# Performance work log

Hardware: AMD Instinct MI355X
Metric: run time of the kernel (lower is better)

The kernel has to match this reference:

```python
import jax, jax.numpy as jnp
import numpy as np

# ---- static skeleton configuration ----
TOPOLOGY = [[0,1],[1,2],[2,3],[3,4],[0,5],[5,6],[6,7],[7,8],[0,9],[9,10],[10,11],[11,12],
            [12,13],[13,14],[12,15],[15,16],[16,17],[17,18],[18,19],[12,20],[20,21],[21,22],[22,23],[23,24]]
NEIGHBOUR_LIST = [[0,1,2,4,5,8,9,24],[0,1,2,3,4,8],[0,1,2,3],[1,2,3],[0,1,4,5,6,8,9,24],[0,4,5,6,7,8],
                  [4,5,6,7],[5,6,7],[0,1,4,5,8,9,10,24],[0,4,8,9,10,11],[8,9,10,11,12,14,19],
                  [9,10,11,12,13,14,15,19,20],[10,11,12,13,14,15,19,20],[11,12,13,14,19],
                  [10,11,12,13,14,15,16,19,20],[11,12,14,15,16,17,19],[14,15,16,17,18],[15,16,17,18],
                  [16,17,18],[10,11,12,13,14,15,19,20,21],[11,12,14,19,20,21,22],[19,20,21,22,23],
                  [20,21,22,23],[21,22,23],[0,4,8,24]]
JOINT_NUM, IN_C, OUT_C, K, STRIDE, PAD = 25, 200, 400, 3, 2, 1
GN_GROUPS, GN_EPS = 10, 1e-5

def build_mask(nbr_list, in_c, out_c, joint_num, k):
    cin, cout = in_c // joint_num, out_c // joint_num
    m = np.zeros((out_c, in_c, k), np.float32)
    for i, nbr in enumerate(nbr_list):
        cols = [j * cin + c for j in nbr for c in range(cin)]
        m[i * cout:(i + 1) * cout, cols, :] = 1.0
    return jnp.asarray(m)

def build_pool(edges, cpe):
    edge_num = len(edges) + 1
    deg = {}
    for a, b in edges:
        deg[a] = deg.get(a, 0) + 1; deg[b] = deg.get(b, 0) + 1
    seq_list = []
    def find_seq(j, seq):
        if deg[j] > 2 and j != 0:
            seq_list.append(seq); seq = []
        if deg[j] == 1:
            seq_list.append(seq); return
        for idx, (a, b) in enumerate(edges):
            if a == j:
                find_seq(b, seq + [idx])
    find_seq(0, [])
    pooling_list = []
    for seq in seq_list:
        if len(seq) % 2 == 1:
            pooling_list.append([seq[0]]); seq = seq[1:]
        for i in range(0, len(seq), 2):
            pooling_list.append([seq[i], seq[i + 1]])
    pooling_list.append([edge_num - 1])
    W = np.zeros((len(pooling_list) * cpe, edge_num * cpe), np.float32)
    for i, pair in enumerate(pooling_list):
        for j in pair:
            W[i * cpe:(i + 1) * cpe, j * cpe:(j + 1) * cpe] += np.eye(cpe, dtype=np.float32) / len(pair)
    return jnp.asarray(W)

MASK0 = build_mask(NEIGHBOUR_LIST, IN_C, IN_C, JOINT_NUM, K)    # extra conv in->in
MASK1 = build_mask(NEIGHBOUR_LIST, IN_C, OUT_C, JOINT_NUM, K)   # main conv in->out
MASK_SC = build_mask(NEIGHBOUR_LIST, IN_C, OUT_C, JOINT_NUM, 1) # shortcut k=1
POOL_W = build_pool(TOPOLOGY, OUT_C // JOINT_NUM)               # [224, 400]

def conv1d(x, w, b, stride, pad):
    if pad > 0:
        x = jnp.pad(x, ((0, 0), (0, 0), (pad, pad)), mode='reflect')
    y = jax.lax.conv_general_dilated(x, w, (stride,), 'VALID',
                                     dimension_numbers=('NCH', 'OIH', 'NCH'))
    return y + b[None, :, None]

def group_norm(x, gamma, beta):
    B, C, T = x.shape
    xg = x.reshape(B, GN_GROUPS, C // GN_GROUPS, T)
    mu = xg.mean((2, 3), keepdims=True)
    var = xg.var((2, 3), keepdims=True)
    xn = ((xg - mu) * jax.lax.rsqrt(var + GN_EPS)).reshape(B, C, T)
    return xn * gamma[None, :, None] + beta[None, :, None]

def prelu(x, a):
    return jnp.where(x >= 0, x, a[0] * x)

def setup_inputs() -> dict:
    key = jax.random.key(0)
    ks = jax.random.split(key, 8)
    return {
        'x': jax.random.normal(ks[0], (16, IN_C, 8192), jnp.float32),
        'w0': jax.random.normal(ks[1], (IN_C, IN_C, K), jnp.float32) * 0.05,
        'b0': jax.random.normal(ks[2], (IN_C,), jnp.float32) * 0.05,
        'a0': jnp.full((1,), 0.25, jnp.float32),
        'w1': jax.random.normal(ks[3], (OUT_C, IN_C, K), jnp.float32) * 0.05,
        'b1': jax.random.normal(ks[4], (OUT_C,), jnp.float32) * 0.05,
        'gn_gamma': jnp.ones((OUT_C,), jnp.float32),
        'gn_beta': jnp.zeros((OUT_C,), jnp.float32),
        'ws': jax.random.normal(ks[5], (OUT_C, IN_C, 1), jnp.float32) * 0.05,
        'bs': jax.random.normal(ks[6], (OUT_C,), jnp.float32) * 0.05,
        'a1': jnp.full((1,), 0.25, jnp.float32),
    }

def reference(x, w0, b0, a0, w1, b1, gn_gamma, gn_beta, ws, bs, a1):
    # residual branch: extra SkeletonConv + PReLU, SkeletonConv (stride 2), GroupNorm
    h = conv1d(x, w0 * MASK0, b0, 1, PAD)
    h = prelu(h, a0)
    h = conv1d(h, w1 * MASK1, b1, STRIDE, PAD)
    h = group_norm(h, gn_gamma, gn_beta)
    # shortcut: masked 1x1 conv, stride 2
    s = conv1d(x, ws * MASK_SC, bs, STRIDE, 0)
    out = h + s                                   # [B, 400, 4096]
    out = jnp.einsum('nc,bct->bnt', POOL_W, out)  # SkeletonPool mean -> [B, 224, 4096]
    return prelu(out, a1)
```

## Files before the change

### kernel.cpp

```cpp
#include <hip/hip_runtime.h>

#define BATCH 16
#define CIN   200
#define T1    8192
#define COUTC 400
#define TT2   4096
#define NJ    25
#define NGROUP 10
#define CPG   40
#define NPOOL 14
#define CROWB 528

typedef __attribute__((ext_vector_type(8))) short bf16x8;
typedef __attribute__((ext_vector_type(4))) float f32x4;

__constant__ int NBR_OFF[NJ + 1] = {0,8,14,18,21,29,35,39,42,50,56,63,72,80,85,94,101,106,110,113,122,129,134,138,141,145};
__constant__ int NBR[145] = {
 0,1,2,4,5,8,9,24,
 0,1,2,3,4,8,
 0,1,2,3,
 1,2,3,
 0,1,4,5,6,8,9,24,
 0,4,5,6,7,8,
 4,5,6,7,
 5,6,7,
 0,1,4,5,8,9,10,24,
 0,4,8,9,10,11,
 8,9,10,11,12,14,19,
 9,10,11,12,13,14,15,19,20,
 10,11,12,13,14,15,19,20,
 11,12,13,14,19,
 10,11,12,13,14,15,16,19,20,
 11,12,14,15,16,17,19,
 14,15,16,17,18,
 15,16,17,18,
 16,17,18,
 10,11,12,13,14,15,19,20,21,
 11,12,14,19,20,21,22,
 19,20,21,22,23,
 20,21,22,23,
 21,22,23,
 0,4,8,24};
__constant__ int PAIR_A[NPOOL] = {0,2,4,6,8,10,12,14,15,17,19,20,22,24};
__constant__ int PAIR_B[NPOOL] = {1,3,5,7,9,11,13,-1,16,18,-1,21,23,-1};
__constant__ int JSPLIT8[9] = {0,3,6,9,12,15,18,21,25};
__constant__ int QPB[4] = {0,4,7,10};
__constant__ int QPE[4] = {4,7,10,14};
__constant__ int PUOFF[15] = {0,9,13,22,26,35,45,53,62,70,74,83,91,95,99};
__constant__ int PU[99] = {
 0,1,2,3,4,5,8,9,24,
 0,1,2,3,
 0,1,4,5,6,7,8,9,24,
 4,5,6,7,
 0,1,4,5,8,9,10,11,24,
 8,9,10,11,12,13,14,15,19,20,
 10,11,12,13,14,15,19,20,
 10,11,12,13,14,15,16,19,20,
 11,12,14,15,16,17,18,19,
 15,16,17,18,
 10,11,12,13,14,15,19,20,21,
 11,12,14,19,20,21,22,23,
 20,21,22,23,
 0,4,8,24};
__constant__ int PNMF[NPOOL] = {7,3,7,3,7,8,6,7,6,3,7,6,3,3};
__constant__ int FB0[NPOOL]  = {0,7,10,17,20,27,35,41,48,54,57,64,70,73};
__constant__ int FRAG_P[76] = {
 0,0,0,0,0,0,0, 1,1,1, 2,2,2,2,2,2,2, 3,3,3, 4,4,4,4,4,4,4, 5,5,5,5,5,5,5,5,
 6,6,6,6,6,6, 7,7,7,7,7,7,7, 8,8,8,8,8,8, 9,9,9, 10,10,10,10,10,10,10,
 11,11,11,11,11,11, 12,12,12, 13,13,13};
__constant__ int NSF[NJ] = {2,2,1,1,2,2,1,1,2,2,2,3,2,2,3,2,2,1,1,3,2,2,1,1,1};
__constant__ int FBS[NJ] = {0,2,4,5,6,8,10,11,12,14,16,18,21,23,25,28,30,32,33,34,37,39,41,42,43};
__constant__ int FRAG_SJ[44] = {
 0,0, 1,1, 2, 3, 4,4, 5,5, 6, 7, 8,8, 9,9, 10,10, 11,11,11, 12,12, 13,13,
 14,14,14, 15,15, 16,16, 17, 18, 19,19,19, 20,20, 21,21, 22, 23, 24};
#define NF1   (NJ * 7)
#define DSC_SC   304
#define DSC_C1   480
#define DSC_TOT  (DSC_C1 + NF1 * 4)

__device__ __forceinline__ unsigned bfround(float f) {
    unsigned u = __builtin_bit_cast(unsigned, f);
    return (u + 0x7FFFu + ((u >> 16) & 1u)) >> 16;
}
__device__ __forceinline__ unsigned packbf(float lo, float hi) {
    return bfround(lo) | (bfround(hi) << 16);
}
__device__ __forceinline__ float bflo(unsigned u) { return __builtin_bit_cast(float, u << 16); }
__device__ __forceinline__ float bfhi(unsigned u) { return __builtin_bit_cast(float, u & 0xFFFF0000u); }

__global__ void prep_all(const float* __restrict__ w1, const float* __restrict__ w0,
                         const float* __restrict__ wsc,
                         unsigned short* __restrict__ wA1, unsigned short* __restrict__ wA0,
                         unsigned short* __restrict__ wAs, int* __restrict__ dsc)
{
    const int bid = blockIdx.x;
    if (bid < NF1) {
        const int f  = bid;
        const int jo = f / 7;
        const int mf = f - jo * 7;
        const int off = NBR_OFF[jo];
        const int deg = NBR_OFF[jo + 1] - off;
        for (int e = threadIdx.x; e < 512; e += 256) {
            int lane = e >> 3, j = e & 7;
            int m = lane & 15, kb = lane >> 4;
            int c8 = mf * 4 + kb;
            float v = 0.f;
            if (c8 < 3 * deg) {
                int tap = (c8 >= 2 * deg) ? 2 : ((c8 >= deg) ? 1 : 0);
                int nbr_i = c8 - tap * deg;
                int ci = NBR[off + nbr_i] * 8 + j;
                v = w1[(size_t)(jo * 16 + m) * 600 + ci * 3 + tap];
            }
            wA1[(size_t)f * 512 + e] = (unsigned short)bfround(v);
        }
    } else if (bid < NF1 + 76) {
        const int f  = bid - NF1;
        const int p  = FRAG_P[f];
        const int mf = f - FB0[p];
        const int puo = PUOFF[p];
        const int u   = PUOFF[p + 1] - puo;
        for (int e = threadIdx.x; e < 512; e += 256) {
            int lane = e >> 3, j = e & 7;
            int m = lane & 15, kb = lane >> 4;
            int c8 = mf * 4 + kb;
            int jm = (m < 8) ? PAIR_A[p] : PAIR_B[p];
            float v = 0.f;
            if (c8 < 3 * u && jm >= 0) {
                int tap = (c8 >= 2 * u) ? 2 : ((c8 >= u) ? 1 : 0);
                int ni  = c8 - tap * u;
                int nbr = PU[puo + ni];
                int offj = NBR_OFF[jm], degj = NBR_OFF[jm + 1] - offj;
                bool mem = false;
                for (int s = 0; s < degj; ++s) mem = mem || (NBR[offj + s] == nbr);
                if (mem) {
                    int ci = nbr * 8 + j;
                    v = w0[(size_t)(jm * 8 + (m & 7)) * 600 + ci * 3 + tap];
                }
            }
            wA0[(size_t)f * 512 + e] = (unsigned short)bfround(v);
        }
    } else if (bid < NF1 + 76 + 44) {
        const int f  = bid - NF1 - 76;
        const int jo = FRAG_SJ[f];
        const int mf = f - FBS[jo];
        const int off = NBR_OFF[jo];
        const int deg = NBR_OFF[jo + 1] - off;
        for (int e = threadIdx.x; e < 512; e += 256) {
            int lane = e >> 3, j = e & 7;
            int m = lane & 15, kb = lane >> 4;
            int c8 = mf * 4 + kb;
            float v = 0.f;
            if (c8 < deg) {
                int ci = NBR[off + c8] * 8 + j;
                v = wsc[(size_t)(jo * 16 + m) * 200 + ci];
            }
            wAs[(size_t)f * 512 + e] = (unsigned short)bfround(v);
        }
    } else {
        for (int e = threadIdx.x; e < DSC_TOT; e += 256) {
            if (e < DSC_SC) {
                int f = e >> 2, q = e & 3;
                int p = FRAG_P[f], mf = f - FB0[p];
                int puo = PUOFF[p], u = PUOFF[p + 1] - puo;
                int c8 = mf * 4 + q;
                int tp = 0, ni = 0;
                if (c8 < 3 * u) {
                    tp = (c8 >= 2 * u) ? 2 : ((c8 >= u) ? 1 : 0);
                    ni = c8 - tp * u;
                }
                dsc[e] = (tp << 12) | (PU[puo + ni] * 16);
            } else if (e < DSC_C1) {
                int e2 = e - DSC_SC;
                int f = e2 >> 2, q = e2 & 3;
                int jo = FRAG_SJ[f], mf = f - FBS[jo];
                int off = NBR_OFF[jo], deg = NBR_OFF[jo + 1] - off;
                int c8 = mf * 4 + q;
                int ni = (c8 < deg) ? c8 : deg - 1;
                dsc[e] = NBR[off + ni] * 16;
            } else {
                int e2 = e - DSC_C1;
                int f = e2 >> 2, q = e2 & 3;
                int jo = f / 7, mf = f - jo * 7;
                int off = NBR_OFF[jo], deg = NBR_OFF[jo + 1] - off;
                int c8 = mf * 4 + q;
                int tp = 0, ni = 0;
                if (c8 < 3 * deg) {
                    tp = (c8 >= 2 * deg) ? 2 : ((c8 >= deg) ? 1 : 0);
                    ni = c8 - tp * deg;
                }
                int rowd = (tp == 1) ? 33 : (tp >> 1);
                dsc[e] = rowd * CROWB + NBR[off + ni] * 16;
            }
        }
    }
}

__global__ __launch_bounds__(512) void conv0s_mfma(
    const float* __restrict__ x, const unsigned short* __restrict__ wA0,
    const unsigned short* __restrict__ wAs, const int* __restrict__ dsc,
    const float* __restrict__ b0, const float* __restrict__ a0,
    const float* __restrict__ bsc,
    unsigned short* __restrict__ h0T, unsigned short* __restrict__ sbu)
{
    __shared__ __align__(16) unsigned short xs[66 * 264];
    __shared__ int dl[DSC_C1];
    __shared__ float b0l[CIN], bscl[COUTC];
    const int b   = blockIdx.y;
    const int t0  = blockIdx.x * 64;
    const int tid = threadIdx.x;

    for (int i = tid; i < DSC_C1; i += 512) dl[i] = dsc[i];
    for (int i = tid; i < CIN; i += 512) b0l[i] = b0[i];
    for (int i = tid; i < COUTC; i += 512) bscl[i] = bsc[i];

    const float* xb = x + (size_t)b * CIN * T1;
    for (int e = tid; e < (CIN / 8) * 16; e += 512) {
        int c8i = e >> 4, k = e & 15;
        const float* xc = xb + (size_t)(8 * c8i) * T1 + t0 + 4 * k;
        float4 v0 = *(const float4*)(xc);
        float4 v1 = *(const float4*)(xc + T1);
        float4 v2 = *(const float4*)(xc + 2 * T1);
        float4 v3 = *(const float4*)(xc + 3 * T1);
        float4 v4 = *(const float4*)(xc + 4 * T1);
        float4 v5 = *(const float4*)(xc + 5 * T1);
        float4 v6 = *(const float4*)(xc + 6 * T1);
        float4 v7 = *(const float4*)(xc + 7 * T1);
        char* base = (char*)xs + 16 * c8i + (4 * k + 1) * CROWB;
        *(uint4*)(base) = make_uint4(packbf(v0.x, v1.x), packbf(v2.x, v3.x),
                                     packbf(v4.x, v5.x), packbf(v6.x, v7.x));
        *(uint4*)(base + CROWB) = make_uint4(packbf(v0.y, v1.y), packbf(v2.y, v3.y),
                                             packbf(v4.y, v5.y), packbf(v6.y, v7.y));
        *(uint4*)(base + 2 * CROWB) = make_uint4(packbf(v0.z, v1.z), packbf(v2.z, v3.z),
                                                 packbf(v4.z, v5.z), packbf(v6.z, v7.z));
        *(uint4*)(base + 3 * CROWB) = make_uint4(packbf(v0.w, v1.w), packbf(v2.w, v3.w),
                                                 packbf(v4.w, v5.w), packbf(v6.w, v7.w));
    }
    for (int e = tid; e < 2 * CIN; e += 512) {
        int c = e >> 1, h = e & 1;
        int t = h ? (t0 + 64) : (t0 - 1);
        t = (t < 0) ? 1 : ((t >= T1) ? (2 * T1 - 2 - t) : t);
        float v = xb[(size_t)c * T1 + t];
        *(unsigned short*)((char*)xs + (h ? 65 : 0) * CROWB + 2 * c) = (unsigned short)bfround(v);
    }
    __syncthreads();

    const int w = tid >> 6, lane = tid & 63;
    const int q = lane >> 4, n = lane & 15;
    const float alpha = a0[0];
    const int ws2 = w & 1, wh = w >> 1;
    const int rA = ws2 * 32 + n;
    char* xsb = (char*)xs + rA * CROWB;

    unsigned h0k[4][2][2];
    for (int p = QPB[wh], pl = 0; p < QPE[wh]; ++p, ++pl) {
        const int fb = FB0[p], nmf = PNMF[p];
        const unsigned short* wAb = wA0 + (size_t)fb * 512;
        f32x4 acc0 = {0.f, 0.f, 0.f, 0.f};
        f32x4 acc1 = {0.f, 0.f, 0.f, 0.f};
        int i1 = (nmf > 1) ? 1 : 0;
        bf16x8 af0 = *(const bf16x8*)(wAb + (size_t)lane * 8);
        int d = dl[fb * 4 + q];
        bf16x8 b0v = *(const bf16x8*)(xsb + (d >> 12) * CROWB + (d & 0xFFF));
        bf16x8 b1v = *(const bf16x8*)(xsb + (d >> 12) * CROWB + (d & 0xFFF) + 16 * CROWB);
        bf16x8 af1 = *(const bf16x8*)(wAb + ((size_t)i1 * 64 + lane) * 8);
        d = dl[(fb + i1) * 4 + q];
        bf16x8 b0n = *(const bf16x8*)(xsb + (d >> 12) * CROWB + (d & 0xFFF));
        bf16x8 b1n = *(const bf16x8*)(xsb + (d >> 12) * CROWB + (d & 0xFFF) + 16 * CROWB);
        for (int mf = 0; mf < nmf; ++mf) {
            int m2 = (mf + 2 < nmf) ? mf + 2 : nmf - 1;
            bf16x8 a2 = *(const bf16x8*)(wAb + ((size_t)m2 * 64 + lane) * 8);
            d = dl[(fb + m2) * 4 + q];
            bf16x8 b02 = *(const bf16x8*)(xsb + (d >> 12) * CROWB + (d & 0xFFF));
            bf16x8 b12 = *(const bf16x8*)(xsb + (d >> 12) * CROWB + (d & 0xFFF) + 16 * CROWB);
            acc0 = __builtin_amdgcn_mfma_f32_16x16x32_bf16(af0, b0v, acc0, 0, 0, 0);
            acc1 = __builtin_amdgcn_mfma_f32_16x16x32_bf16(af0, b1v, acc1, 0, 0, 0);
            af0 = af1; af1 = a2;
            b0v = b0n; b0n = b02;
            b1v = b1n; b1n = b12;
        }
        int jm = (q < 2) ? PAIR_A[p] : PAIR_B[p];
        if (jm >= 0) {
            int ocb = (q & 1) * 4;
            float bb0 = b0l[jm * 8 + ocb + 0], bb1 = b0l[jm * 8 + ocb + 1];
            float bb2 = b0l[jm * 8 + ocb + 2], bb3 = b0l[jm * 8 + ocb + 3];
            float v0 = acc0[0] + bb0; v0 = (v0 >= 0.f) ? v0 : alpha * v0;
            float v1 = acc0[1] + bb1; v1 = (v1 >= 0.f) ? v1 : alpha * v1;
            float v2 = acc0[2] + bb2; v2 = (v2 >= 0.f) ? v2 : alpha * v2;
            float v3 = acc0[3] + bb3; v3 = (v3 >= 0.f) ? v3 : alpha * v3;
            h0k[pl][0][0] = packbf(v0, v1); h0k[pl][0][1] = packbf(v2, v3);
            v0 = acc1[0] + bb0; v0 = (v0 >= 0.f) ? v0 : alpha * v0;
            v1 = acc1[1] + bb1; v1 = (v1 >= 0.f) ? v1 : alpha * v1;
            v2 = acc1[2] + bb2; v2 = (v2 >= 0.f) ? v2 : alpha * v2;
            v3 = acc1[3] + bb3; v3 = (v3 >= 0.f) ? v3 : alpha * v3;
            h0k[pl][1][0] = packbf(v0, v1); h0k[pl][1][1] = packbf(v2, v3);
        }
    }

    for (int jo = w; jo < NJ; jo += 8) {
        const int fb = FBS[jo], nsf = NSF[jo];
        const unsigned short* wAb = wAs + (size_t)fb * 512;
        const int dbase = DSC_SC + fb * 4 + q;
        char* rb0 = (char*)xs + (2 * n + 1) * CROWB;
        f32x4 acc0 = {0.f, 0.f, 0.f, 0.f};
        f32x4 acc1 = {0.f, 0.f, 0.f, 0.f};
        int i1 = (nsf > 1) ? 1 : 0;
        bf16x8 af0 = *(const bf16x8*)(wAb + (size_t)lane * 8);
        int d = dl[dbase];
        bf16x8 b0v = *(const bf16x8*)(rb0 + d);
        bf16x8 b1v = *(const bf16x8*)(rb0 + d + 32 * CROWB);
        bf16x8 af1 = *(const bf16x8*)(wAb + ((size_t)i1 * 64 + lane) * 8);
        d = dl[dbase + i1 * 4];
        bf16x8 b0n = *(const bf16x8*)(rb0 + d);
        bf16x8 b1n = *(const bf16x8*)(rb0 + d + 32 * CROWB);
        for (int mf = 0; mf < nsf; ++mf) {
            int m2 = (mf + 2 < nsf) ? mf + 2 : nsf - 1;
            bf16x8 a2 = *(const bf16x8*)(wAb + ((size_t)m2 * 64 + lane) * 8);
            d = dl[dbase + m2 * 4];
            bf16x8 b02 = *(const bf16x8*)(rb0 + d);
            bf16x8 b12 = *(const bf16x8*)(rb0 + d + 32 * CROWB);
            acc0 = __builtin_amdgcn_mfma_f32_16x16x32_bf16(af0, b0v, acc0, 0, 0, 0);
            acc1 = __builtin_amdgcn_mfma_f32_16x16x32_bf16(af0, b1v, acc1, 0, 0, 0);
            af0 = af1; af1 = a2;
            b0v = b0n; b0n = b02;
            b1v = b1n; b1n = b12;
        }
        unsigned short* sp = sbu + ((size_t)b * COUTC + jo * 16 + q * 4) * TT2 + (t0 >> 1) + n;
#pragma unroll
        for (int r = 0; r < 4; ++r) {
            float bsv = bscl[jo * 16 + q * 4 + r];
            sp[(size_t)r * TT2]      = (unsigned short)bfround(acc0[r] + bsv);
            sp[(size_t)r * TT2 + 16] = (unsigned short)bfround(acc1[r] + bsv);
        }
    }

    __syncthreads();
    for (int p = QPB[wh], pl = 0; p < QPE[wh]; ++p, ++pl) {
        int jm = (q < 2) ? PAIR_A[p] : PAIR_B[p];
        if (jm >= 0) {
            int cb = (jm * 8 + (q & 1) * 4) * 2;
            *(uint2*)((char*)xs + rA * CROWB + cb)        = make_uint2(h0k[pl][0][0], h0k[pl][0][1]);
            *(uint2*)((char*)xs + (rA + 16) * CROWB + cb) = make_uint2(h0k[pl][1][0], h0k[pl][1][1]);
        }
    }
    __syncthreads();
    unsigned short* ho = h0T + ((size_t)b * T1 + t0 + w * 8) * CIN;
    for (int e = lane; e < 8 * 25; e += 64) {
        int row = e / 25, k = e - row * 25;
        uint4 u = *(const uint4*)((char*)xs + (w * 8 + row) * CROWB + 16 * k);
        *(uint4*)(ho + (size_t)row * CIN + 8 * k) = u;
    }
}

__global__ __launch_bounds__(512) void conv1_mfma(
    const unsigned short* __restrict__ h0T, const unsigned short* __restrict__ wA,
    const int* __restrict__ dsc, const float* __restrict__ b1,
    unsigned short* __restrict__ h1u, float* __restrict__ part)
{
    __shared__ __align__(16) unsigned short xs[65 * 264];
    __shared__ int dl1[NF1 * 4];
    __shared__ float biasl[COUTC];
    const int b   = blockIdx.y;
    const int t20 = blockIdx.x * 32;
    const int tid = threadIdx.x;

    for (int i = tid; i < NF1 * 4; i += 512) dl1[i] = dsc[DSC_C1 + i];
    for (int i = tid; i < COUTC; i += 512) biasl[i] = b1[i];

    const unsigned short* hTb = h0T + (size_t)b * T1 * CIN;
    for (int e = tid; e < 65 * 25; e += 512) {
        int row = e / 25, k = e - row * 25;
        int p = (row < 33) ? (2 * t20 - 1 + 2 * row) : (2 * t20 + 2 * (row - 33));
        if (p < 0) p = 1;
        uint4 u = *(const uint4*)(hTb + (size_t)p * CIN + 8 * k);
        *(uint4*)((char*)xs + row * CROWB + 16 * k) = u;
    }
    __syncthreads();

    const int w = tid >> 6, lane = tid & 63;
    const int q = lane >> 4, n = lane & 15;
    const int j0 = JSPLIT8[w], j1 = JSPLIT8[w + 1];
    const int t2gA = t20 + n, t2gB = t20 + 16 + n;
    char* xsb = (char*)xs + n * CROWB;

    for (int jo = j0; jo < j1; ++jo) {
        const unsigned short* wAb = wA + (size_t)(jo * 7) * 512;
        const int dbase = jo * 28 + q;
        f32x4 acc0 = {0.f, 0.f, 0.f, 0.f};
        f32x4 acc1 = {0.f, 0.f, 0.f, 0.f};
#pragma unroll
        for (int mf = 0; mf < 7; ++mf) {
            bf16x8 a = *(const bf16x8*)(wAb + ((size_t)mf * 64 + lane) * 8);
            int d = dl1[dbase + mf * 4];
            bf16x8 bb0 = *(const bf16x8*)(xsb + d);
            bf16x8 bb1 = *(const bf16x8*)(xsb + d + 16 * CROWB);
            acc0 = __builtin_amdgcn_mfma_f32_16x16x32_bf16(a, bb0, acc0, 0, 0, 0);
            acc1 = __builtin_amdgcn_mfma_f32_16x16x32_bf16(a, bb1, acc1, 0, 0, 0);
        }

        float s = 0.f, ss = 0.f;
        unsigned short* hout = h1u + ((size_t)b * COUTC + jo * 16) * TT2;
#pragma unroll
        for (int r = 0; r < 4; ++r) {
            int oc = q * 4 + r;
            float bv = biasl[jo * 16 + oc];
            float v0 = acc0[r] + bv;
            float v1 = acc1[r] + bv;
            s += v0 + v1; ss += v0 * v0 + v1 * v1;
            hout[(size_t)oc * TT2 + t2gA] = (unsigned short)bfround(v0);
            hout[(size_t)oc * TT2 + t2gB] = (unsigned short)bfround(v1);
        }
        for (int o2 = 1; o2 < 32; o2 <<= 1) {
            s  += __shfl_xor(s, o2, 64);
            ss += __shfl_xor(ss, o2, 64);
        }
        if ((lane & 31) == 0) {
            int half = lane >> 5;
            size_t o = (((size_t)b * 50 + jo * 2 + half) * 128 + blockIdx.x) * 2;
            part[o] = s; part[o + 1] = ss;
        }
    }
}

__global__ __launch_bounds__(256) void gn_final2(const float* __restrict__ part,
                                                 float* __restrict__ stats)
{
    const int bg = blockIdx.x;
    const int b = bg / NGROUP, g = bg % NGROUP;
    float s = 0.f, ss = 0.f;
    for (int k = threadIdx.x; k < 5 * 128; k += 256) {
        int sb = k >> 7, slot = k & 127;
        size_t o = (((size_t)b * 50 + g * 5 + sb) * 128 + slot) * 2;
        s += part[o]; ss += part[o + 1];
    }
    for (int o2 = 32; o2; o2 >>= 1) {
        s  += __shfl_down(s, o2, 64);
        ss += __shfl_down(ss, o2, 64);
    }
    __shared__ float rs[4], rss[4];
    const int lane = threadIdx.x & 63, wv = threadIdx.x >> 6;
    if (lane == 0) { rs[wv] = s; rss[wv] = ss; }
    __syncthreads();
    if (threadIdx.x == 0) {
        float S  = rs[0] + rs[1] + rs[2] + rs[3];
        float SS = rss[0] + rss[1] + rss[2] + rss[3];
        const float invN = 1.0f / (float)(CPG * TT2);
        float mean = S * invN;
        float var  = SS * invN - mean * mean;
        stats[bg * 2]     = mean;
        stats[bg * 2 + 1] = rsqrtf(var + 1e-5f);
    }
}

__global__ void gn_coef(const float* __restrict__ stats, const float* __restrict__ gamma,
                        const float* __restrict__ beta, float* __restrict__ AB)
{
    int idx = blockIdx.x * 256 + threadIdx.x;
    if (idx < BATCH * COUTC) {
        int b = idx / COUTC; int ch = idx - b * COUTC;
        int g = ch / CPG;
        float m = stats[(b * NGROUP + g) * 2];
        float r = stats[(b * NGROUP + g) * 2 + 1];
        float A = r * gamma[ch];
        AB[(size_t)idx * 2]     = A;
        AB[(size_t)idx * 2 + 1] = beta[ch] - m * A;
    }
}

__global__ __launch_bounds__(256) void final2pb(
    const unsigned* __restrict__ h1b, const unsigned* __restrict__ sb,
    const float* __restrict__ AB, const float* __restrict__ a1,
    float* __restrict__ outb)
{
    const int n     = blockIdx.y >> 1;
    const int chalf = blockIdx.y & 1;
    const int b     = blockIdx.z;
    const int tid   = threadIdx.x;
    const int t0    = (blockIdx.x * 256 + tid) * 4;

    int js[2];
    js[0] = PAIR_A[n];
    const int jb = PAIR_B[n];
    const int L = (jb >= 0) ? 2 : 1;
    js[1] = (jb >= 0) ? jb : js[0];

    __shared__ float Al[2][8], Bl[2][8];
    if (tid < 16) {
        int ji = tid >> 3, c8 = tid & 7;
        int ch = js[ji] * 16 + chalf * 8 + c8;
        Al[ji][c8] = AB[((size_t)b * COUTC + ch) * 2];
        Bl[ji][c8] = AB[((size_t)b * COUTC + ch) * 2 + 1];
    }
    __syncthreads();

    const float alpha = a1[0];
    const float invL  = (L == 2) ? 0.5f : 1.0f;

    float acc[8][4];
#pragma unroll
    for (int c = 0; c < 8; ++c)
#pragma unroll
        for (int i = 0; i < 4; ++i) acc[c][i] = 0.f;

    for (int ji = 0; ji < L; ++ji) {
        const int jc0 = js[ji] * 16 + chalf * 8;
#pragma unroll
        for (int c = 0; c < 8; ++c) {
            size_t rowoff = ((size_t)b * COUTC + jc0 + c) * (TT2 / 2) + t0 / 2;
            uint2 hv = *(const uint2*)(h1b + rowoff);
            uint2 sv = *(const uint2*)(sb + rowoff);
            float A = Al[ji][c], Bc = Bl[ji][c];
            acc[c][0] += bflo(hv.x) * A + Bc + bflo(sv.x);
            acc[c][1] += bfhi(hv.x) * A + Bc + bfhi(sv.x);
            acc[c][2] += bflo(hv.y) * A + Bc + bflo(sv.y);
            acc[c][3] += bfhi(hv.y) * A + Bc + bfhi(sv.y);
        }
    }

    float* ob = outb + ((size_t)b * 224 + n * 16 + chalf * 8) * TT2 + t0;
#pragma unroll
    for (int c = 0; c < 8; ++c) {
        float4 o;
#pragma unroll
        for (int i = 0; i < 4; ++i) {
            float v = acc[c][i] * invL;
            ((float*)&o)[i] = (v >= 0.f) ? v : alpha * v;
        }
        *(float4*)(ob + (size_t)c * TT2) = o;
    }
}

extern "C" void kernel_launch(void* const* d_in, const int* in_sizes, int n_in,
                              void* d_out, int out_size, void* d_ws, size_t ws_size,
                              hipStream_t stream) {
    const float* x     = (const float*)d_in[0];
    const float* w0    = (const float*)d_in[1];
    const float* b0    = (const float*)d_in[2];
    const float* a0    = (const float*)d_in[3];
    const float* w1    = (const float*)d_in[4];
    const float* b1    = (const float*)d_in[5];
    const float* gamma = (const float*)d_in[6];
    const float* beta  = (const float*)d_in[7];
    const float* wsc   = (const float*)d_in[8];
    const float* bsc   = (const float*)d_in[9];
    const float* a1    = (const float*)d_in[10];
    float* out = (float*)d_out;

    const size_t NB = (size_t)BATCH * CIN * T1;
    unsigned short* h0T  = (unsigned short*)d_ws;
    unsigned short* sbu  = h0T + NB;
    unsigned short* h1u  = sbu + NB;
    unsigned short* wA1  = h1u + NB;
    unsigned short* wA0p = wA1 + (size_t)NF1 * 512;
    unsigned short* wAsp = wA0p + (size_t)76 * 512;
    int* dsc     = (int*)(wAsp + (size_t)44 * 512);
    float* part  = (float*)(dsc + DSC_TOT);
    float* stats = part + (size_t)BATCH * 50 * 128 * 2;
    float* AB    = stats + BATCH * NGROUP * 2;

    prep_all<<<dim3(NF1 + 76 + 44 + 1), 256, 0, stream>>>(w1, w0, wsc, wA1, wA0p, wAsp, dsc);
    conv0s_mfma<<<dim3(T1 / 64, BATCH), 512, 0, stream>>>(x, wA0p, wAsp, dsc, b0, a0, bsc, h0T, sbu);
    conv1_mfma<<<dim3(TT2 / 32, BATCH), 512, 0, stream>>>(h0T, wA1, dsc, b1, h1u, part);
    gn_final2<<<dim3(BATCH * NGROUP), 256, 0, stream>>>(part, stats);
    gn_coef<<<dim3(25), 256, 0, stream>>>(stats, gamma, beta, AB);
    final2pb<<<dim3(TT2 / 1024, NPOOL * 2, BATCH), 256, 0, stream>>>((const unsigned*)h1u,
                                                                     (const unsigned*)sbu, AB, a1, out);
}
```

Baseline: 154.3 us.

## Have each wave compute all 64 time rows for a load-balanced set of pool groups

The first conv stage used to give each wave 32 time rows and a contiguous range of pool groups. Now each wave covers all 64 rows with four accumulators, so each weight fragment loaded from global memory feeds four MFMAs instead of two. Pool groups are assigned through a reordered table (one or two groups per wave) chosen to balance MFMA counts across the eight waves. The deep register prefetch of B fragments is replaced by a one-step A prefetch with direct LDS reads, which raises register use and may expose more LDS latency.

After: 148.9 us. 3.5% less time.

```diff
diff --git a/kernel.cpp b/kernel.cpp
--- a/kernel.cpp
+++ b/kernel.cpp
@@ -44,8 +44,8 @@
 __constant__ int PAIR_A[NPOOL] = {0,2,4,6,8,10,12,14,15,17,19,20,22,24};
 __constant__ int PAIR_B[NPOOL] = {1,3,5,7,9,11,13,-1,16,18,-1,21,23,-1};
 __constant__ int JSPLIT8[9] = {0,3,6,9,12,15,18,21,25};
-__constant__ int QPB[4] = {0,4,7,10};
-__constant__ int QPE[4] = {4,7,10,14};
+__constant__ int POOL_ORD[14] = {8,11, 0,1, 2,3, 4,9, 10,12, 6,13, 5, 7};
+__constant__ int GB8[9] = {0,2,4,6,8,10,12,13,14};
 __constant__ int PUOFF[15] = {0,9,13,22,26,35,45,53,62,70,74,83,91,95,99};
 __constant__ int PU[99] = {
  0,1,2,3,4,5,8,9,24,
@@ -247,52 +247,49 @@
     const int w = tid >> 6, lane = tid & 63;
     const int q = lane >> 4, n = lane & 15;
     const float alpha = a0[0];
-    const int ws2 = w & 1, wh = w >> 1;
-    const int rA = ws2 * 32 + n;
-    char* xsb = (char*)xs + rA * CROWB;
-
-    unsigned h0k[4][2][2];
-    for (int p = QPB[wh], pl = 0; p < QPE[wh]; ++p, ++pl) {
+    char* xsb = (char*)xs + n * CROWB;
+
+    unsigned h0k[2][4][2];
+    const int g0 = GB8[w], g1 = GB8[w + 1];
+    for (int gi = g0, pl = 0; gi < g1; ++gi, ++pl) {
+        const int p = POOL_ORD[gi];
         const int fb = FB0[p], nmf = PNMF[p];
         const unsigned short* wAb = wA0 + (size_t)fb * 512;
         f32x4 acc0 = {0.f, 0.f, 0.f, 0.f};
         f32x4 acc1 = {0.f, 0.f, 0.f, 0.f};
-        int i1 = (nmf > 1) ? 1 : 0;
-        bf16x8 af0 = *(const bf16x8*)(wAb + (size_t)lane * 8);
-        int d = dl[fb * 4 + q];
-        bf16x8 b0v = *(const bf16x8*)(xsb + (d >> 12) * CROWB + (d & 0xFFF));
-        bf16x8 b1v = *(const bf16x8*)(xsb + (d >> 12) * CROWB + (d & 0xFFF) + 16 * CROWB);
-        bf16x8 af1 = *(const bf16x8*)(wAb + ((size_t)i1 * 64 + lane) * 8);
-        d = dl[(fb + i1) * 4 + q];
-        bf16x8 b0n = *(const bf16x8*)(xsb + (d >> 12) * CROWB + (d & 0xFFF));
-        bf16x8 b1n = *(const bf16x8*)(xsb + (d >> 12) * CROWB + (d & 0xFFF) + 16 * CROWB);
+        f32x4 acc2 = {0.f, 0.f, 0.f, 0.f};
+        f32x4 acc3 = {0.f, 0.f, 0.f, 0.f};
+        bf16x8 aCur = *(const bf16x8*)(wAb + (size_t)lane * 8);
         for (int mf = 0; mf < nmf; ++mf) {
-            int m2 = (mf + 2 < nmf) ? mf + 2 : nmf - 1;
-            bf16x8 a2 = *(const bf16x8*)(wAb + ((size_t)m2 * 64 + lane) * 8);
-            d = dl[(fb + m2) * 4 + q];
-            bf16x8 b02 = *(const bf16x8*)(xsb + (d >> 12) * CROWB + (d & 0xFFF));
-            bf16x8 b12 = *(const bf16x8*)(xsb + (d >> 12) * CROWB + (d & 0xFFF) + 16 * CROWB);
-            acc0 = __builtin_amdgcn_mfma_f32_16x16x32_bf16(af0, b0v, acc0, 0, 0, 0);
-            acc1 = __builtin_amdgcn_mfma_f32_16x16x32_bf16(af0, b1v, acc1, 0, 0, 0);
-            af0 = af1; af1 = a2;
-            b0v = b0n; b0n = b02;
-            b1v = b1n; b1n = b12;
+            int m2 = (mf + 1 < nmf) ? mf + 1 : mf;
+            bf16x8 aNxt = *(const bf16x8*)(wAb + ((size_t)m2 * 64 + lane) * 8);
+            int d = dl[(fb + mf) * 4 + q];
+            char* bp = xsb + (d >> 12) * CROWB + (d & 0xFFF);
+            bf16x8 B0 = *(const bf16x8*)(bp);
+            bf16x8 B1 = *(const bf16x8*)(bp + 16 * CROWB);
+            bf16x8 B2 = *(const bf16x8*)(bp + 32 * CROWB);
+            bf16x8 B3 = *(const bf16x8*)(bp + 48 * CROWB);
+            acc0 = __builtin_amdgcn_mfma_f32_16x16x32_bf16(aCur, B0, acc0, 0, 0, 0);
+            acc1 = __builtin_amdgcn_mfma_f32_16x16x32_bf16(aCur, B1, acc1, 0, 0, 0);
+            acc2 = __builtin_amdgcn_mfma_f32_16x16x32_bf16(aCur, B2, acc2, 0, 0, 0);
+            acc3 = __builtin_amdgcn_mfma_f32_16x16x32_bf16(aCur, B3, acc3, 0, 0, 0);
+            aCur = aNxt;
         }
         int jm = (q < 2) ? PAIR_A[p] : PAIR_B[p];
         if (jm >= 0) {
             int ocb = (q & 1) * 4;
             float bb0 = b0l[jm * 8 + ocb + 0], bb1 = b0l[jm * 8 + ocb + 1];
             float bb2 = b0l[jm * 8 + ocb + 2], bb3 = b0l[jm * 8 + ocb + 3];
-            float v0 = acc0[0] + bb0; v0 = (v0 >= 0.f) ? v0 : alpha * v0;
-            float v1 = acc0[1] + bb1; v1 = (v1 >= 0.f) ? v1 : alpha * v1;
-            float v2 = acc0[2] + bb2; v2 = (v2 >= 0.f) ? v2 : alpha * v2;
-            float v3 = acc0[3] + bb3; v3 = (v3 >= 0.f) ? v3 : alpha * v3;
-            h0k[pl][0][0] = packbf(v0, v1); h0k[pl][0][1] = packbf(v2, v3);
-            v0 = acc1[0] + bb0; v0 = (v0 >= 0.f) ? v0 : alpha * v0;
-            v1 = acc1[1] + bb1; v1 = (v1 >= 0.f) ? v1 : alpha * v1;
-            v2 = acc1[2] + bb2; v2 = (v2 >= 0.f) ? v2 : alpha * v2;
-            v3 = acc1[3] + bb3; v3 = (v3 >= 0.f) ? v3 : alpha * v3;
-            h0k[pl][1][0] = packbf(v0, v1); h0k[pl][1][1] = packbf(v2, v3);
+            f32x4 aa[4] = {acc0, acc1, acc2, acc3};
+#pragma unroll
+            for (int s = 0; s < 4; ++s) {
+                float v0 = aa[s][0] + bb0; v0 = (v0 >= 0.f) ? v0 : alpha * v0;
+                float v1 = aa[s][1] + bb1; v1 = (v1 >= 0.f) ? v1 : alpha * v1;
+                float v2 = aa[s][2] + bb2; v2 = (v2 >= 0.f) ? v2 : alpha * v2;
+                float v3 = aa[s][3] + bb3; v3 = (v3 >= 0.f) ? v3 : alpha * v3;
+                h0k[pl][s][0] = packbf(v0, v1);
+                h0k[pl][s][1] = packbf(v2, v3);
+            }
         }
     }
 
@@ -334,12 +331,15 @@
     }
 
     __syncthreads();
-    for (int p = QPB[wh], pl = 0; p < QPE[wh]; ++p, ++pl) {
+    for (int gi = g0, pl = 0; gi < g1; ++gi, ++pl) {
+        int p = POOL_ORD[gi];
         int jm = (q < 2) ? PAIR_A[p] : PAIR_B[p];
         if (jm >= 0) {
             int cb = (jm * 8 + (q & 1) * 4) * 2;
-            *(uint2*)((char*)xs + rA * CROWB + cb)        = make_uint2(h0k[pl][0][0], h0k[pl][0][1]);
-            *(uint2*)((char*)xs + (rA + 16) * CROWB + cb) = make_uint2(h0k[pl][1][0], h0k[pl][1][1]);
+#pragma unroll
+            for (int s = 0; s < 4; ++s)
+                *(uint2*)((char*)xs + (16 * s + n) * CROWB + cb) =
+                    make_uint2(h0k[pl][s][0], h0k[pl][s][1]);
         }
     }
     __syncthreads();
```
